# Performance work log

Measured on AMD Instinct MI355X. Metric: run time of the kernel, lower is better.

## Reference

```python
import jax, jax.numpy as jnp
import numpy as np

TAU = 0.5

def _projection(z, W1, b1, W2, b2):
    h = jax.nn.elu(z @ W1.T + b1)
    return h @ W2.T + b2

def _normalize(x, eps=1e-12):
    n = jnp.linalg.norm(x, axis=1, keepdims=True)
    return x / jnp.maximum(n, eps)

def setup_inputs() -> dict:
    key = jax.random.key(0)
    k = jax.random.split(key, 6)
    N, D, P = 8192, 256, 256
    s = 1.0 / np.sqrt(D)
    return {
        "z1": jax.random.normal(k[0], (N, D), jnp.float32),
        "z2": jax.random.normal(k[1], (N, D), jnp.float32),
        "W1": jax.random.normal(k[2], (P, D), jnp.float32) * s,
        "b1": jnp.zeros((P,), jnp.float32),
        "W2": jax.random.normal(k[3], (D, P), jnp.float32) * s,
        "b2": jnp.zeros((D,), jnp.float32),
    }

def reference(z1, z2, W1, b1, W2, b2):
    h1 = _projection(z1, W1, b1, W2, b2)
    h2 = _projection(z2, W1, b1, W2, b2)
    n1 = _normalize(h1)
    n2 = _normalize(h2)
    f11 = jnp.exp((n1 @ n1.T) / TAU)  # [N,N]
    f22 = jnp.exp((n2 @ n2.T) / TAU)
    f12 = jnp.exp((n1 @ n2.T) / TAU)
    d12 = jnp.diagonal(f12)
    l1 = -jnp.log(d12 / (f11.sum(1) + f12.sum(1) - jnp.diagonal(f11)))
    # sim(h2,h1) = f12.T: diag same, row-sum = column-sum of f12
    l2 = -jnp.log(d12 / (f22.sum(1) + f12.sum(0) - jnp.diagonal(f22)))
    return (l1 + l2) * 0.5
```

## Files before the change

kernel.cpp:

```cpp
#include <hip/hip_runtime.h>
#include <hip/hip_bf16.h>
#include <hip/hip_fp8.h>
#include <stdint.h>

#define Nn 8192
#define Dd 256
#define TWO_N 16384
#define INV_TAU 2.0f

typedef unsigned short u16;
typedef unsigned char u8;
typedef long long i64;
typedef __bf16 bf16x8 __attribute__((ext_vector_type(8)));
typedef float f32x4 __attribute__((ext_vector_type(4)));

typedef const __attribute__((address_space(1))) void* gas_ptr;
typedef __attribute__((address_space(3))) void* las_ptr;

__device__ __forceinline__ void async_copy16(const void* g, void* l) {
  __builtin_amdgcn_global_load_lds((gas_ptr)g, (las_ptr)l, 16, 0, 0);
}

__device__ __forceinline__ u16 f2bf(float x) {
  uint32_t u = __float_as_uint(x);
  u = u + 0x7fffu + ((u >> 16) & 1u);
  return (u16)(u >> 16);
}
__device__ __forceinline__ float bf2f(u16 u) {
  return __uint_as_float(((uint32_t)u) << 16);
}

__global__ void cast_all(const float* __restrict__ z1, const float* __restrict__ z2,
                         const float* __restrict__ W1, const float* __restrict__ W2,
                         u16* __restrict__ Zb, u16* __restrict__ W1b, u16* __restrict__ W2b) {
  int i = blockIdx.x * 256 + threadIdx.x;
  const float4* src; ushort4* dst; int off;
  if (i < 524288)       { src = (const float4*)z1; dst = (ushort4*)Zb;                      off = i; }
  else if (i < 1048576) { src = (const float4*)z2; dst = (ushort4*)(Zb + (size_t)Nn * Dd);  off = i - 524288; }
  else if (i < 1064960) { src = (const float4*)W1; dst = (ushort4*)W1b;                     off = i - 1048576; }
  else                  { src = (const float4*)W2; dst = (ushort4*)W2b;                     off = i - 1064960; }
  float4 v = src[off];
  ushort4 o;
  o.x = f2bf(v.x); o.y = f2bf(v.y); o.z = f2bf(v.z); o.w = f2bf(v.w);
  dst[off] = o;
}

__global__ __launch_bounds__(256)
void mfma_gemm1(const u16* __restrict__ A, const u16* __restrict__ B,
                const float* __restrict__ bias, u16* __restrict__ outp) {
  __shared__ __bf16 sA[128 * 64];
  __shared__ __bf16 sB[128 * 64];
  const int i0 = blockIdx.x * 128;
  const int j0 = blockIdx.y * 128;
  const int t = threadIdx.x;
  const int lane = t & 63, wave = t >> 6;
  const int wm = (wave >> 1) * 64, wn = (wave & 1) * 64;
  const int fr = lane >> 4, fc = lane & 15;
  const int sw = fc & 7;

  f32x4 acc[4][4];
#pragma unroll
  for (int a = 0; a < 4; a++)
#pragma unroll
    for (int b = 0; b < 4; b++) acc[a][b] = (f32x4){0.f, 0.f, 0.f, 0.f};

  const u16* Ag = A + (size_t)i0 * 256;
  const u16* Bg = B + (size_t)j0 * 256;

  for (int k0 = 0; k0 < 256; k0 += 64) {
    __syncthreads();
#pragma unroll
    for (int it = 0; it < 4; ++it) {
      int c = t + 256 * it;
      int row = c >> 3;
      int kc = ((c & 7) ^ (row & 7)) * 8;
      async_copy16(Ag + (size_t)row * 256 + k0 + kc, (void*)&sA[c * 8]);
      async_copy16(Bg + (size_t)row * 256 + k0 + kc, (void*)&sB[c * 8]);
    }
    __syncthreads();
#pragma unroll
    for (int ks = 0; ks < 2; ++ks) {
      bf16x8 af[4], bfr[4];
#pragma unroll
      for (int mi = 0; mi < 4; mi++)
        af[mi] = *(const bf16x8*)&sA[(wm + mi * 16 + fc) * 64 + (((ks * 4 + fr) ^ sw) * 8)];
#pragma unroll
      for (int ni = 0; ni < 4; ni++)
        bfr[ni] = *(const bf16x8*)&sB[(wn + ni * 16 + fc) * 64 + (((ks * 4 + fr) ^ sw) * 8)];
#pragma unroll
      for (int mi = 0; mi < 4; mi++)
#pragma unroll
        for (int ni = 0; ni < 4; ni++)
          acc[mi][ni] = __builtin_amdgcn_mfma_f32_16x16x32_bf16(af[mi], bfr[ni], acc[mi][ni], 0, 0, 0);
    }
  }

#pragma unroll
  for (int mi = 0; mi < 4; mi++) {
#pragma unroll
    for (int ni = 0; ni < 4; ni++) {
      int col = j0 + wn + ni * 16 + fc;
      float bv = bias[col];
#pragma unroll
      for (int r = 0; r < 4; r++) {
        int row = i0 + wm + mi * 16 + fr * 4 + r;
        float v = acc[mi][ni][r] + bv;
        v = v > 0.f ? v : (__expf(v) - 1.f);
        outp[(size_t)row * 256 + col] = f2bf(v);
      }
    }
  }
}

__global__ __launch_bounds__(256)
void gemm2_norm(const u16* __restrict__ A, const u16* __restrict__ B,
                const float* __restrict__ bias, u16* __restrict__ Mb,
                u8* __restrict__ Mf8, float* __restrict__ snorm,
                float* __restrict__ rsum) {
  __shared__ __bf16 sA[128 * 64];
  __shared__ __bf16 sB[256 * 64];
  const int i0 = blockIdx.x * 128;
  const int t = threadIdx.x;
  const int lane = t & 63, wave = t >> 6;
  const int wm = (wave >> 1) * 64, wn = (wave & 1) * 128;
  const int fr = lane >> 4, fc = lane & 15;
  const int sw = fc & 7;

  if (t < 128) rsum[i0 + t] = 0.f;

  f32x4 acc[4][8];
#pragma unroll
  for (int a = 0; a < 4; a++)
#pragma unroll
    for (int b = 0; b < 8; b++) acc[a][b] = (f32x4){0.f, 0.f, 0.f, 0.f};

  const u16* Ag = A + (size_t)i0 * 256;

  for (int k0 = 0; k0 < 256; k0 += 64) {
    __syncthreads();
#pragma unroll
    for (int it = 0; it < 4; ++it) {
      int c = t + 256 * it;
      int row = c >> 3;
      int kc = ((c & 7) ^ (row & 7)) * 8;
      async_copy16(Ag + (size_t)row * 256 + k0 + kc, (void*)&sA[c * 8]);
    }
#pragma unroll
    for (int it = 0; it < 8; ++it) {
      int c = t + 256 * it;
      int row = c >> 3;
      int kc = ((c & 7) ^ (row & 7)) * 8;
      async_copy16(B + (size_t)row * 256 + k0 + kc, (void*)&sB[c * 8]);
    }
    __syncthreads();
#pragma unroll
    for (int ks = 0; ks < 2; ++ks) {
      bf16x8 af[4], bfr[8];
#pragma unroll
      for (int mi = 0; mi < 4; mi++)
        af[mi] = *(const bf16x8*)&sA[(wm + mi * 16 + fc) * 64 + (((ks * 4 + fr) ^ sw) * 8)];
#pragma unroll
      for (int ni = 0; ni < 8; ni++)
        bfr[ni] = *(const bf16x8*)&sB[(wn + ni * 16 + fc) * 64 + (((ks * 4 + fr) ^ sw) * 8)];
#pragma unroll
      for (int mi = 0; mi < 4; mi++)
#pragma unroll
        for (int ni = 0; ni < 8; ni++)
          acc[mi][ni] = __builtin_amdgcn_mfma_f32_16x16x32_bf16(af[mi], bfr[ni], acc[mi][ni], 0, 0, 0);
    }
  }

  float bv[8];
#pragma unroll
  for (int ni = 0; ni < 8; ni++) bv[ni] = bias[wn + ni * 16 + fc];

  __syncthreads();
  float* red = (float*)sA;

#pragma unroll
  for (int mi = 0; mi < 4; mi++) {
    float ssq[4] = {0.f, 0.f, 0.f, 0.f};
#pragma unroll
    for (int ni = 0; ni < 8; ni++)
#pragma unroll
      for (int r = 0; r < 4; r++) {
        float v = acc[mi][ni][r] + bv[ni];
        acc[mi][ni][r] = v;
        ssq[r] += v * v;
      }
#pragma unroll
    for (int r = 0; r < 4; r++) {
      float v = ssq[r];
#pragma unroll
      for (int off = 1; off < 16; off <<= 1) v += __shfl_xor(v, off, 16);
      if (fc == 0) red[(wm + mi * 16 + fr * 4 + r) * 2 + (wn >> 7)] = v;
    }
  }
  __syncthreads();

  float* red2 = red + 256;
#pragma unroll
  for (int mi = 0; mi < 4; mi++) {
    float ssq2[4] = {0.f, 0.f, 0.f, 0.f};
#pragma unroll
    for (int r = 0; r < 4; r++) {
      int row = wm + mi * 16 + fr * 4 + r;
      float ss = red[row * 2] + red[row * 2 + 1];
      float rn = 1.f / fmaxf(sqrtf(ss), 1e-12f);
#pragma unroll
      for (int ni = 0; ni < 8; ni++) {
        float v = acc[mi][ni][r] * rn;
        Mb[(size_t)(i0 + row) * 256 + wn + ni * 16 + fc] = f2bf(v);
        __hip_fp8_e4m3 q(v);
        Mf8[(size_t)(i0 + row) * 256 + wn + ni * 16 + fc] = q.__x;
        float fv = (float)q;
        ssq2[r] += fv * fv;
      }
    }
#pragma unroll
    for (int r = 0; r < 4; r++) {
      float v = ssq2[r];
#pragma unroll
      for (int off = 1; off < 16; off <<= 1) v += __shfl_xor(v, off, 16);
      if (fc == 0) red2[(wm + mi * 16 + fr * 4 + r) * 2 + (wn >> 7)] = v;
    }
  }
  __syncthreads();
  if (t < 128) snorm[i0 + t] = red2[t * 2] + red2[t * 2 + 1];
}

__global__ __launch_bounds__(256, 3)
void gram_sym(const u8* __restrict__ Mf8, float* __restrict__ rsum) {
  __shared__ u8 sA8[128 * 256];
  __shared__ u8 sB8[2][128 * 64];
  const int t = threadIdx.x;
  const int lane = t & 63, wave = t >> 6;
  const int wm = (wave >> 1) * 64, wn = (wave & 1) * 64;
  const int fr = lane >> 4, fc = lane & 15;

  int f = 2111 - blockIdx.x;
  int b = 0;
  while (f >= 2 * (b + 1) * (b + 2)) ++b;
  int rem = f - 2 * b * (b + 1);
  int r = rem / (b + 1);
  int q = rem - r * (b + 1);
  int k = 4 * b + 1 + r;
  const int i_t = 128 - k;
  const int jt0 = i_t + 4 * q;
  const int L = min(4, k - 4 * q);

  const int i0 = i_t * 128;
  const u8* Ag = Mf8 + (size_t)i0 * 256;

#pragma unroll
  for (int it = 0; it < 8; ++it) {
    int c = t + 256 * it;
    int row = c >> 4, pos = c & 15;
    int g = (pos & 8) | ((pos & 7) ^ (row & 7));
    async_copy16(Ag + (size_t)row * 256 + g * 16, (void*)&sA8[c * 16]);
  }
  {
    const u8* Bg = Mf8 + (size_t)jt0 * 128 * 256;
#pragma unroll
    for (int it = 0; it < 2; ++it) {
      int c = t + 256 * it;
      int row = c >> 2, pos = c & 3;
      int g = pos ^ ((row + (row >> 2)) & 3);
      async_copy16(Bg + (size_t)row * 256 + g * 16, (void*)&sB8[0][c * 16]);
    }
  }

  float rowacc[4][4];
#pragma unroll
  for (int a = 0; a < 4; a++)
#pragma unroll
    for (int rr = 0; rr < 4; rr++) rowacc[a][rr] = 0.f;

  f32x4 acc[4][4];
#pragma unroll
  for (int a = 0; a < 4; a++)
#pragma unroll
    for (int bb = 0; bb < 4; bb++) acc[a][bb] = (f32x4){0.f, 0.f, 0.f, 0.f};

  const int totalc = L * 4;
  for (int cc = 0; cc < totalc; ++cc) {
    __syncthreads();

    if (cc + 1 < totalc) {
      const u8* Bgn = Mf8 + (size_t)(jt0 + ((cc + 1) >> 2)) * 128 * 256;
      const int k0n = ((cc + 1) & 3) * 64;
      u8* dst = sB8[(cc + 1) & 1];
#pragma unroll
      for (int it = 0; it < 2; ++it) {
        int c = t + 256 * it;
        int row = c >> 2, pos = c & 3;
        int g = pos ^ ((row + (row >> 2)) & 3);
        async_copy16(Bgn + (size_t)row * 256 + k0n + g * 16, (void*)&dst[c * 16]);
      }
    }

    const int kch = cc & 3;
    const u8* sB = sB8[cc & 1];
#pragma unroll
    for (int ks = 0; ks < 2; ++ks) {
      i64 af[4], bf[4];
#pragma unroll
      for (int mi = 0; mi < 4; mi++) {
        int row = wm + mi * 16 + fc;
        int g16 = kch * 4 + ks * 2 + (fr >> 1);
        int sg = (g16 & 8) | ((g16 & 7) ^ (row & 7));
        af[mi] = *(const i64*)&sA8[row * 256 + sg * 16 + (fr & 1) * 8];
      }
#pragma unroll
      for (int ni = 0; ni < 4; ni++) {
        int row = wn + ni * 16 + fc;
        int g16 = ks * 2 + (fr >> 1);
        int sg = g16 ^ ((row + (row >> 2)) & 3);
        bf[ni] = *(const i64*)&sB[row * 64 + sg * 16 + (fr & 1) * 8];
      }
#pragma unroll
      for (int mi = 0; mi < 4; mi++)
#pragma unroll
        for (int ni = 0; ni < 4; ni++)
          acc[mi][ni] = __builtin_amdgcn_mfma_f32_16x16x32_fp8_fp8(af[mi], bf[ni], acc[mi][ni], 0, 0, 0);
    }

    if ((cc & 3) == 3) {
      const int j_t = jt0 + (cc >> 2);
      const int j0 = j_t * 128;
      float colp[4] = {0.f, 0.f, 0.f, 0.f};
#pragma unroll
      for (int mi = 0; mi < 4; mi++) {
#pragma unroll
        for (int ni = 0; ni < 4; ni++) {
          float e0 = __expf(acc[mi][ni][0] * INV_TAU);
          float e1 = __expf(acc[mi][ni][1] * INV_TAU);
          float e2 = __expf(acc[mi][ni][2] * INV_TAU);
          float e3 = __expf(acc[mi][ni][3] * INV_TAU);
          rowacc[mi][0] += e0; rowacc[mi][1] += e1;
          rowacc[mi][2] += e2; rowacc[mi][3] += e3;
          colp[ni] += e0 + e1 + e2 + e3;
          acc[mi][ni] = (f32x4){0.f, 0.f, 0.f, 0.f};
        }
      }
      if (j_t != i_t) {
#pragma unroll
        for (int ni = 0; ni < 4; ni++) {
          float v = colp[ni];
          v += __shfl_xor(v, 16, 64);
          v += __shfl_xor(v, 32, 64);
          if (fr == 0) atomicAdd(&rsum[j0 + wn + ni * 16 + fc], v);
        }
      }
    }
  }

#pragma unroll
  for (int mi = 0; mi < 4; mi++) {
#pragma unroll
    for (int rr = 0; rr < 4; rr++) {
      float v = rowacc[mi][rr];
#pragma unroll
      for (int off = 1; off < 16; off <<= 1) v += __shfl_xor(v, off, 16);
      rowacc[mi][rr] = v;
    }
  }
  if (fc == 0) {
#pragma unroll
    for (int mi = 0; mi < 4; mi++) {
      int rbase = i0 + wm + mi * 16 + fr * 4;
      atomicAdd(&rsum[rbase + 0], rowacc[mi][0]);
      atomicAdd(&rsum[rbase + 1], rowacc[mi][1]);
      atomicAdd(&rsum[rbase + 2], rowacc[mi][2]);
      atomicAdd(&rsum[rbase + 3], rowacc[mi][3]);
    }
  }
}

__global__ void final_loss(const u16* __restrict__ Mb, const float* __restrict__ rsum,
                           const float* __restrict__ snorm, float* __restrict__ out) {
  int i = blockIdx.x * 4 + (threadIdx.x >> 6);
  int lane = threadIdx.x & 63;
  ushort4 ua = ((const ushort4*)(Mb + (size_t)i * 256))[lane];
  ushort4 ub = ((const ushort4*)(Mb + (size_t)(Nn + i) * 256))[lane];
  float d = bf2f(ua.x) * bf2f(ub.x) + bf2f(ua.y) * bf2f(ub.y) +
            bf2f(ua.z) * bf2f(ub.z) + bf2f(ua.w) * bf2f(ub.w);
#pragma unroll
  for (int off = 32; off; off >>= 1) d += __shfl_xor(d, off, 64);
  if (lane == 0) {
    float den1 = rsum[i] - __expf(snorm[i] * INV_TAU);
    float den2 = rsum[Nn + i] - __expf(snorm[Nn + i] * INV_TAU);
    out[i] = 0.5f * (logf(den1) + logf(den2)) - d * INV_TAU;
  }
}

extern "C" void kernel_launch(void* const* d_in, const int* in_sizes, int n_in,
                              void* d_out, int out_size, void* d_ws, size_t ws_size,
                              hipStream_t stream) {
  const float* z1 = (const float*)d_in[0];
  const float* z2 = (const float*)d_in[1];
  const float* W1 = (const float*)d_in[2];
  const float* b1 = (const float*)d_in[3];
  const float* W2 = (const float*)d_in[4];
  const float* b2 = (const float*)d_in[5];
  float* out = (float*)d_out;

  char* ws = (char*)d_ws;
  u16*   Zb    = (u16*)(ws);
  u16*   H1b   = (u16*)(ws + (8u << 20));
  u8*    Mf8   = (u8*)(ws + (16u << 20));
  u16*   W1b   = (u16*)(ws + (20u << 20));
  u16*   W2b   = (u16*)(ws + (20u << 20) + 131072);
  float* rsum  = (float*)(ws + (20u << 20) + 262144);
  float* snorm = (float*)(ws + (20u << 20) + 262144 + 65536);
  u16*   Mb    = Zb;

  cast_all<<<1081344 / 256, 256, 0, stream>>>(z1, z2, W1, W2, Zb, W1b, W2b);

  mfma_gemm1<<<dim3(TWO_N / 128, 2), 256, 0, stream>>>(Zb, W1b, b1, H1b);

  gemm2_norm<<<TWO_N / 128, 256, 0, stream>>>(H1b, W2b, b2, Mb, Mf8, snorm, rsum);

  gram_sym<<<2112, 256, 0, stream>>>(Mf8, rsum);

  final_loss<<<Nn / 4, 256, 0, stream>>>(Mb, rsum, snorm, out);
}
```

Before: 188.4 us.

## Fuse input casts into GEMMs, use K=128 FP8 MFMA, drop bf16 output

Removes the separate cast kernel: both GEMMs now load fp32 inputs and weights and convert them to bf16 while staging into shared memory. The gram kernel switches to the 16x16x128 scaled f8f6f4 MFMA. It keeps the A fragments in registers and double-buffers full 128x256 B tiles, cutting the synchronization rounds per tile from four to one at the cost of lower occupancy (launch bounds 3 to 2). The bf16 normalized-embedding write is dropped, and the final loss computes the positive-pair dot from the fp8 copy instead, which may reduce accuracy of the diagonal term.

After: 181.9 us. -3.4%, faster.

```diff
diff --git a/kernel.cpp b/kernel.cpp
--- a/kernel.cpp
+++ b/kernel.cpp
@@ -4,15 +4,14 @@
 #include <stdint.h>
 
 #define Nn 8192
-#define Dd 256
 #define TWO_N 16384
 #define INV_TAU 2.0f
 
 typedef unsigned short u16;
 typedef unsigned char u8;
-typedef long long i64;
 typedef __bf16 bf16x8 __attribute__((ext_vector_type(8)));
 typedef float f32x4 __attribute__((ext_vector_type(4)));
+typedef int i32x8 __attribute__((ext_vector_type(8)));
 
 typedef const __attribute__((address_space(1))) void* gas_ptr;
 typedef __attribute__((address_space(3))) void* las_ptr;
@@ -26,32 +25,18 @@
   u = u + 0x7fffu + ((u >> 16) & 1u);
   return (u16)(u >> 16);
 }
-__device__ __forceinline__ float bf2f(u16 u) {
-  return __uint_as_float(((uint32_t)u) << 16);
-}
-
-__global__ void cast_all(const float* __restrict__ z1, const float* __restrict__ z2,
-                         const float* __restrict__ W1, const float* __restrict__ W2,
-                         u16* __restrict__ Zb, u16* __restrict__ W1b, u16* __restrict__ W2b) {
-  int i = blockIdx.x * 256 + threadIdx.x;
-  const float4* src; ushort4* dst; int off;
-  if (i < 524288)       { src = (const float4*)z1; dst = (ushort4*)Zb;                      off = i; }
-  else if (i < 1048576) { src = (const float4*)z2; dst = (ushort4*)(Zb + (size_t)Nn * Dd);  off = i - 524288; }
-  else if (i < 1064960) { src = (const float4*)W1; dst = (ushort4*)W1b;                     off = i - 1048576; }
-  else                  { src = (const float4*)W2; dst = (ushort4*)W2b;                     off = i - 1064960; }
-  float4 v = src[off];
-  ushort4 o;
-  o.x = f2bf(v.x); o.y = f2bf(v.y); o.z = f2bf(v.z); o.w = f2bf(v.w);
-  dst[off] = o;
-}
 
 __global__ __launch_bounds__(256)
-void mfma_gemm1(const u16* __restrict__ A, const u16* __restrict__ B,
-                const float* __restrict__ bias, u16* __restrict__ outp) {
+void mfma_gemm1(const float* __restrict__ z1, const float* __restrict__ z2,
+                const float* __restrict__ W1, const float* __restrict__ bias,
+                u16* __restrict__ outp) {
   __shared__ __bf16 sA[128 * 64];
   __shared__ __bf16 sB[128 * 64];
-  const int i0 = blockIdx.x * 128;
+  const int bx = blockIdx.x;
+  const int i0 = bx * 128;
   const int j0 = blockIdx.y * 128;
+  const float* Zsrc = (bx < 64) ? (z1 + (size_t)i0 * 256) : (z2 + (size_t)(i0 - Nn) * 256);
+  const float* Wsrc = W1 + (size_t)j0 * 256;
   const int t = threadIdx.x;
   const int lane = t & 63, wave = t >> 6;
   const int wm = (wave >> 1) * 64, wn = (wave & 1) * 64;
@@ -64,18 +49,25 @@
 #pragma unroll
     for (int b = 0; b < 4; b++) acc[a][b] = (f32x4){0.f, 0.f, 0.f, 0.f};
 
-  const u16* Ag = A + (size_t)i0 * 256;
-  const u16* Bg = B + (size_t)j0 * 256;
-
   for (int k0 = 0; k0 < 256; k0 += 64) {
     __syncthreads();
 #pragma unroll
     for (int it = 0; it < 4; ++it) {
       int c = t + 256 * it;
       int row = c >> 3;
-      int kc = ((c & 7) ^ (row & 7)) * 8;
-      async_copy16(Ag + (size_t)row * 256 + k0 + kc, (void*)&sA[c * 8]);
-      async_copy16(Bg + (size_t)row * 256 + k0 + kc, (void*)&sB[c * 8]);
+      int g = (c & 7) ^ (row & 7);
+      const float* sa = Zsrc + (size_t)row * 256 + k0 + g * 8;
+      float4 a0 = *(const float4*)sa;
+      float4 a1 = *(const float4*)(sa + 4);
+      bf16x8 va = {(__bf16)a0.x, (__bf16)a0.y, (__bf16)a0.z, (__bf16)a0.w,
+                   (__bf16)a1.x, (__bf16)a1.y, (__bf16)a1.z, (__bf16)a1.w};
+      *(bf16x8*)&sA[c * 8] = va;
+      const float* sb = Wsrc + (size_t)row * 256 + k0 + g * 8;
+      float4 b0 = *(const float4*)sb;
+      float4 b1v = *(const float4*)(sb + 4);
+      bf16x8 vb = {(__bf16)b0.x, (__bf16)b0.y, (__bf16)b0.z, (__bf16)b0.w,
+                   (__bf16)b1v.x, (__bf16)b1v.y, (__bf16)b1v.z, (__bf16)b1v.w};
+      *(bf16x8*)&sB[c * 8] = vb;
     }
     __syncthreads();
 #pragma unroll
@@ -113,10 +105,9 @@
 }
 
 __global__ __launch_bounds__(256)
-void gemm2_norm(const u16* __restrict__ A, const u16* __restrict__ B,
-                const float* __restrict__ bias, u16* __restrict__ Mb,
-                u8* __restrict__ Mf8, float* __restrict__ snorm,
-                float* __restrict__ rsum) {
+void gemm2_norm(const u16* __restrict__ A, const float* __restrict__ W2,
+                const float* __restrict__ bias, u8* __restrict__ Mf8,
+                float* __restrict__ snorm, float* __restrict__ rsum) {
   __shared__ __bf16 sA[128 * 64];
   __shared__ __bf16 sB[256 * 64];
   const int i0 = blockIdx.x * 128;
@@ -149,8 +140,13 @@
     for (int it = 0; it < 8; ++it) {
       int c = t + 256 * it;
       int row = c >> 3;
-      int kc = ((c & 7) ^ (row & 7)) * 8;
-      async_copy16(B + (size_t)row * 256 + k0 + kc, (void*)&sB[c * 8]);
+      int g = (c & 7) ^ (row & 7);
+      const float* sb = W2 + (size_t)row * 256 + k0 + g * 8;
+      float4 b0 = *(const float4*)sb;
+      float4 b1v = *(const float4*)(sb + 4);
+      bf16x8 vb = {(__bf16)b0.x, (__bf16)b0.y, (__bf16)b0.z, (__bf16)b0.w,
+                   (__bf16)b1v.x, (__bf16)b1v.y, (__bf16)b1v.z, (__bf16)b1v.w};
+      *(bf16x8*)&sB[c * 8] = vb;
     }
     __syncthreads();
 #pragma unroll
@@ -210,7 +206,6 @@
 #pragma unroll
       for (int ni = 0; ni < 8; ni++) {
         float v = acc[mi][ni][r] * rn;
-        Mb[(size_t)(i0 + row) * 256 + wn + ni * 16 + fc] = f2bf(v);
         __hip_fp8_e4m3 q(v);
         Mf8[(size_t)(i0 + row) * 256 + wn + ni * 16 + fc] = q.__x;
         float fv = (float)q;
@@ -229,10 +224,9 @@
   if (t < 128) snorm[i0 + t] = red2[t * 2] + red2[t * 2 + 1];
 }
 
-__global__ __launch_bounds__(256, 3)
+__global__ __launch_bounds__(256, 2)
 void gram_sym(const u8* __restrict__ Mf8, float* __restrict__ rsum) {
-  __shared__ u8 sA8[128 * 256];
-  __shared__ u8 sB8[2][128 * 64];
+  __shared__ u8 sB8[2][128 * 256];
   const int t = threadIdx.x;
   const int lane = t & 63, wave = t >> 6;
   const int wm = (wave >> 1) * 64, wn = (wave & 1) * 64;
@@ -248,109 +242,105 @@
   const int i_t = 128 - k;
   const int jt0 = i_t + 4 * q;
   const int L = min(4, k - 4 * q);
-
   const int i0 = i_t * 128;
-  const u8* Ag = Mf8 + (size_t)i0 * 256;
-
-#pragma unroll
-  for (int it = 0; it < 8; ++it) {
-    int c = t + 256 * it;
-    int row = c >> 4, pos = c & 15;
-    int g = (pos & 8) | ((pos & 7) ^ (row & 7));
-    async_copy16(Ag + (size_t)row * 256 + g * 16, (void*)&sA8[c * 16]);
-  }
+
   {
     const u8* Bg = Mf8 + (size_t)jt0 * 128 * 256;
 #pragma unroll
-    for (int it = 0; it < 2; ++it) {
+    for (int it = 0; it < 8; ++it) {
       int c = t + 256 * it;
-      int row = c >> 2, pos = c & 3;
-      int g = pos ^ ((row + (row >> 2)) & 3);
+      int row = c >> 4, slot = c & 15;
+      int g = slot ^ (row & 15);
       async_copy16(Bg + (size_t)row * 256 + g * 16, (void*)&sB8[0][c * 16]);
     }
   }
 
+  i32x8 afr[4][2];
+  {
+    const u8* Ag = Mf8 + (size_t)i0 * 256;
+#pragma unroll
+    for (int mi = 0; mi < 4; ++mi) {
+      const u8* rp = Ag + (size_t)(wm + mi * 16 + fc) * 256 + fr * 32;
+#pragma unroll
+      for (int kb = 0; kb < 2; ++kb) {
+        int4 lo = *(const int4*)(rp + kb * 128);
+        int4 hi = *(const int4*)(rp + kb * 128 + 16);
+        afr[mi][kb] = (i32x8){lo.x, lo.y, lo.z, lo.w, hi.x, hi.y, hi.z, hi.w};
+      }
+    }
+  }
+
   float rowacc[4][4];
 #pragma unroll
   for (int a = 0; a < 4; a++)
 #pragma unroll
     for (int rr = 0; rr < 4; rr++) rowacc[a][rr] = 0.f;
 
-  f32x4 acc[4][4];
-#pragma unroll
-  for (int a = 0; a < 4; a++)
-#pragma unroll
-    for (int bb = 0; bb < 4; bb++) acc[a][bb] = (f32x4){0.f, 0.f, 0.f, 0.f};
-
-  const int totalc = L * 4;
-  for (int cc = 0; cc < totalc; ++cc) {
+  for (int jt = 0; jt < L; ++jt) {
+    const int j_t = jt0 + jt;
+    const int j0 = j_t * 128;
+    const u8* sB = &sB8[jt & 1][0];
+
     __syncthreads();
 
-    if (cc + 1 < totalc) {
-      const u8* Bgn = Mf8 + (size_t)(jt0 + ((cc + 1) >> 2)) * 128 * 256;
-      const int k0n = ((cc + 1) & 3) * 64;
-      u8* dst = sB8[(cc + 1) & 1];
-#pragma unroll
-      for (int it = 0; it < 2; ++it) {
+    if (jt + 1 < L) {
+      const u8* Bg = Mf8 + (size_t)(j_t + 1) * 128 * 256;
+      u8* dst = &sB8[(jt + 1) & 1][0];
+#pragma unroll
+      for (int it = 0; it < 8; ++it) {
         int c = t + 256 * it;
-        int row = c >> 2, pos = c & 3;
-        int g = pos ^ ((row + (row >> 2)) & 3);
-        async_copy16(Bgn + (size_t)row * 256 + k0n + g * 16, (void*)&dst[c * 16]);
-      }
-    }
-
-    const int kch = cc & 3;
-    const u8* sB = sB8[cc & 1];
-#pragma unroll
-    for (int ks = 0; ks < 2; ++ks) {
-      i64 af[4], bf[4];
-#pragma unroll
-      for (int mi = 0; mi < 4; mi++) {
-        int row = wm + mi * 16 + fc;
-        int g16 = kch * 4 + ks * 2 + (fr >> 1);
-        int sg = (g16 & 8) | ((g16 & 7) ^ (row & 7));
-        af[mi] = *(const i64*)&sA8[row * 256 + sg * 16 + (fr & 1) * 8];
-      }
+        int row = c >> 4, slot = c & 15;
+        int g = slot ^ (row & 15);
+        async_copy16(Bg + (size_t)row * 256 + g * 16, (void*)&dst[c * 16]);
+      }
+    }
+
+    f32x4 acc[4][4];
+#pragma unroll
+    for (int a = 0; a < 4; a++)
+#pragma unroll
+      for (int bb = 0; bb < 4; bb++) acc[a][bb] = (f32x4){0.f, 0.f, 0.f, 0.f};
+
+#pragma unroll
+    for (int kb = 0; kb < 2; ++kb) {
+      i32x8 bfrag[4];
+#pragma unroll
+      for (int ni = 0; ni < 4; ++ni) {
+        const u8* base = sB + (wn + ni * 16 + fc) * 256;
+        int g0 = kb * 8 + fr * 2;
+        int4 lo = *(const int4*)(base + ((g0 ^ fc) * 16));
+        int4 hi = *(const int4*)(base + (((g0 + 1) ^ fc) * 16));
+        bfrag[ni] = (i32x8){lo.x, lo.y, lo.z, lo.w, hi.x, hi.y, hi.z, hi.w};
+      }
+#pragma unroll
+      for (int mi = 0; mi < 4; mi++)
+#pragma unroll
+        for (int ni = 0; ni < 4; ni++)
+          acc[mi][ni] = __builtin_amdgcn_mfma_scale_f32_16x16x128_f8f6f4(
+              afr[mi][kb], bfrag[ni], acc[mi][ni], 0, 0, 0, 0x7F, 0, 0x7F);
+    }
+
+    float colp[4] = {0.f, 0.f, 0.f, 0.f};
+#pragma unroll
+    for (int mi = 0; mi < 4; mi++) {
 #pragma unroll
       for (int ni = 0; ni < 4; ni++) {
-        int row = wn + ni * 16 + fc;
-        int g16 = ks * 2 + (fr >> 1);
-        int sg = g16 ^ ((row + (row >> 2)) & 3);
-        bf[ni] = *(const i64*)&sB[row * 64 + sg * 16 + (fr & 1) * 8];
-      }
-#pragma unroll
-      for (int mi = 0; mi < 4; mi++)
-#pragma unroll
-        for (int ni = 0; ni < 4; ni++)
-          acc[mi][ni] = __builtin_amdgcn_mfma_f32_16x16x32_fp8_fp8(af[mi], bf[ni], acc[mi][ni], 0, 0, 0);
-    }
-
-    if ((cc & 3) == 3) {
-      const int j_t = jt0 + (cc >> 2);
-      const int j0 = j_t * 128;
-      float colp[4] = {0.f, 0.f, 0.f, 0.f};
-#pragma unroll
-      for (int mi = 0; mi < 4; mi++) {
-#pragma unroll
-        for (int ni = 0; ni < 4; ni++) {
-          float e0 = __expf(acc[mi][ni][0] * INV_TAU);
-          float e1 = __expf(acc[mi][ni][1] * INV_TAU);
-          float e2 = __expf(acc[mi][ni][2] * INV_TAU);
-          float e3 = __expf(acc[mi][ni][3] * INV_TAU);
-          rowacc[mi][0] += e0; rowacc[mi][1] += e1;
-          rowacc[mi][2] += e2; rowacc[mi][3] += e3;
-          colp[ni] += e0 + e1 + e2 + e3;
-          acc[mi][ni] = (f32x4){0.f, 0.f, 0.f, 0.f};
-        }
-      }
-      if (j_t != i_t) {
-#pragma unroll
-        for (int ni = 0; ni < 4; ni++) {
-          float v = colp[ni];
-          v += __shfl_xor(v, 16, 64);
-          v += __shfl_xor(v, 32, 64);
-          if (fr == 0) atomicAdd(&rsum[j0 + wn + ni * 16 + fc], v);
-        }
+        float e0 = __expf(acc[mi][ni][0] * INV_TAU);
+        float e1 = __expf(acc[mi][ni][1] * INV_TAU);
+        float e2 = __expf(acc[mi][ni][2] * INV_TAU);
+        float e3 = __expf(acc[mi][ni][3] * INV_TAU);
+        rowacc[mi][0] += e0; rowacc[mi][1] += e1;
+        rowacc[mi][2] += e2; rowacc[mi][3] += e3;
+        colp[ni] += e0 + e1 + e2 + e3;
+      }
+    }
+    if (j_t != i_t) {
+#pragma unroll
+      for (int ni = 0; ni < 4; ni++) {
+        float v = colp[ni];
+        v += __shfl_xor(v, 16, 64);
+        v += __shfl_xor(v, 32, 64);
+        if (fr == 0) atomicAdd(&rsum[j0 + wn + ni * 16 + fc], v);
       }
     }
   }
@@ -377,14 +367,20 @@
   }
 }
 
-__global__ void final_loss(const u16* __restrict__ Mb, const float* __restrict__ rsum,
+__global__ void final_loss(const u8* __restrict__ Mf8, const float* __restrict__ rsum,
                            const float* __restrict__ snorm, float* __restrict__ out) {
   int i = blockIdx.x * 4 + (threadIdx.x >> 6);
   int lane = threadIdx.x & 63;
-  ushort4 ua = ((const ushort4*)(Mb + (size_t)i * 256))[lane];
-  ushort4 ub = ((const ushort4*)(Mb + (size_t)(Nn + i) * 256))[lane];
-  float d = bf2f(ua.x) * bf2f(ub.x) + bf2f(ua.y) * bf2f(ub.y) +
-            bf2f(ua.z) * bf2f(ub.z) + bf2f(ua.w) * bf2f(ub.w);
+  unsigned int ua = ((const unsigned int*)(Mf8 + (size_t)i * 256))[lane];
+  unsigned int ub = ((const unsigned int*)(Mf8 + (size_t)(Nn + i) * 256))[lane];
+  float d = 0.f;
+#pragma unroll
+  for (int e = 0; e < 4; ++e) {
+    __hip_fp8_e4m3 qa, qb;
+    qa.__x = (ua >> (8 * e)) & 0xFF;
+    qb.__x = (ub >> (8 * e)) & 0xFF;
+    d += (float)qa * (float)qb;
+  }
 #pragma unroll
   for (int off = 32; off; off >>= 1) d += __shfl_xor(d, off, 64);
   if (lane == 0) {
@@ -406,22 +402,16 @@
   float* out = (float*)d_out;
 
   char* ws = (char*)d_ws;
-  u16*   Zb    = (u16*)(ws);
-  u16*   H1b   = (u16*)(ws + (8u << 20));
-  u8*    Mf8   = (u8*)(ws + (16u << 20));
-  u16*   W1b   = (u16*)(ws + (20u << 20));
-  u16*   W2b   = (u16*)(ws + (20u << 20) + 131072);
-  float* rsum  = (float*)(ws + (20u << 20) + 262144);
-  float* snorm = (float*)(ws + (20u << 20) + 262144 + 65536);
-  u16*   Mb    = Zb;
-
-  cast_all<<<1081344 / 256, 256, 0, stream>>>(z1, z2, W1, W2, Zb, W1b, W2b);
-
-  mfma_gemm1<<<dim3(TWO_N / 128, 2), 256, 0, stream>>>(Zb, W1b, b1, H1b);
-
-  gemm2_norm<<<TWO_N / 128, 256, 0, stream>>>(H1b, W2b, b2, Mb, Mf8, snorm, rsum);
+  u16*   H1b   = (u16*)(ws);
+  u8*    Mf8   = (u8*)(ws + (8u << 20));
+  float* rsum  = (float*)(ws + (12u << 20));
+  float* snorm = (float*)(ws + (12u << 20) + 65536);
+
+  mfma_gemm1<<<dim3(TWO_N / 128, 2), 256, 0, stream>>>(z1, z2, W1, b1, H1b);
+
+  gemm2_norm<<<TWO_N / 128, 256, 0, stream>>>(H1b, W2, b2, Mf8, snorm, rsum);
 
   gram_sym<<<2112, 256, 0, stream>>>(Mf8, rsum);
 
-  final_loss<<<Nn / 4, 256, 0, stream>>>(Mb, rsum, snorm, out);
-}
+  final_loss<<<Nn / 4, 256, 0, stream>>>(Mf8, rsum, snorm, out);
+}
```
